# Performance work log

Measured on AMD Instinct MI355X. Metric: run time of the kernel, lower is better.

The kernel has to match this reference:

```python
import jax, jax.numpy as jnp
import numpy as np

EPS = 1e-15
FEAT = 128
HALF = FEAT // 2
N_RBF = 20
CUTOFF = 5.0
NUM_CONV = 3
N_ATOMS = 10000
N_EDGES = 160000
N_Z = 100


def setup_inputs() -> dict:
    key = jax.random.key(0)
    ks = iter(jax.random.split(key, 40))

    def W(shape):
        fan_in = shape[-2] if len(shape) > 1 else 1
        return (jax.random.normal(next(ks), shape, jnp.float32) / np.sqrt(fan_in)).astype(jnp.float32)

    # graph
    xyz = jax.random.normal(next(ks), (N_ATOMS, 3), jnp.float32)
    z = jax.random.randint(next(ks), (N_ATOMS,), 0, N_Z)
    src = jax.random.randint(next(ks), (N_EDGES,), 0, N_ATOMS)
    off = jax.random.randint(next(ks), (N_EDGES,), 1, N_ATOMS)
    nbr_list = jnp.stack([src, (src + off) % N_ATOMS], axis=1)  # directed, no self-loops

    L = NUM_CONV
    inp = dict(
        xyz=xyz, z=z, nbr_list=nbr_list,
        embed=W((N_Z, FEAT)),
        msg_w1=W((L, FEAT, FEAT)), msg_b1=jnp.zeros((L, FEAT), jnp.float32),
        msg_w2=W((L, FEAT, 3 * FEAT)), msg_b2=jnp.zeros((L, 3 * FEAT), jnp.float32),
        dist_w=W((L, N_RBF, 3 * FEAT)), dist_b=jnp.zeros((L, 3 * FEAT), jnp.float32),
        upd_u=W((L, FEAT, FEAT)), upd_v=W((L, FEAT, FEAT)),
        upd_w1=W((L, 2 * FEAT, FEAT)), upd_b1=jnp.zeros((L, FEAT), jnp.float32),
        upd_w2=W((L, FEAT, 3 * FEAT)), upd_b2=jnp.zeros((L, 3 * FEAT), jnp.float32),
        ero_w1=W((FEAT, HALF)), ero_b1=jnp.zeros((HALF,), jnp.float32),
        ero_w2=W((HALF, 1)), ero_b2=jnp.zeros((1,), jnp.float32),
    )
    return inp


def _painn_forces(xyz, z, nbr_list, embed,
                  msg_w1, msg_b1, msg_w2, msg_b2, dist_w, dist_b,
                  upd_u, upd_v, upd_w1, upd_b1, upd_w2, upd_b2,
                  ero_w1, ero_b1, ero_w2, ero_b2):
    N = z.shape[0]
    i, j = nbr_list[:, 0], nbr_list[:, 1]
    r_ij = xyz[j] - xyz[i]                               # [E,3]
    dist = jnp.sqrt(jnp.sum(r_ij * r_ij + EPS, axis=-1))  # [E]
    unit = r_ij / dist[:, None]
    # radial basis: sin(n*pi*d/cutoff)/d, cosine cutoff envelope
    k_n = jnp.arange(1, N_RBF + 1, dtype=jnp.float32) * (np.pi / CUTOFF)
    rbf = jnp.sin(k_n * dist[:, None]) / dist[:, None]   # [E,n_rbf]
    env = jnp.where(dist < CUTOFF,
                    0.5 * (jnp.cos(np.pi * dist / CUTOFF) + 1.0), 0.0)  # [E]

    s = embed[z]                                         # [N,F]
    v = jnp.zeros((N, FEAT, 3), s.dtype)                 # [N,F,3]

    for l in range(NUM_CONV):
        # --- message block ---
        w_s = (rbf @ dist_w[l] + dist_b[l]) * env[:, None]                 # [E,3F]
        phi = jax.nn.silu(s @ msg_w1[l] + msg_b1[l]) @ msg_w2[l] + msg_b2[l]  # [N,3F]
        inv = (phi[j] * w_s).reshape(-1, 3, FEAT)                           # [E,3,F]
        dv_ij = inv[:, 0, :][..., None] * v[j] + inv[:, 2, :][..., None] * unit[:, None, :]
        ds_ij = inv[:, 1, :]
        s = s + jax.ops.segment_sum(ds_ij, i, num_segments=N)
        v = v + jax.ops.segment_sum(dv_ij, i, num_segments=N)
        # --- update block ---
        u_v = jnp.einsum('nfc,fg->ngc', v, upd_u[l])                        # [N,F,3]
        v_v = jnp.einsum('nfc,fg->ngc', v, upd_v[l])
        v_v_norm = jnp.sqrt(jnp.sum(v_v * v_v, axis=-1) + EPS)              # [N,F]
        s_stack = jnp.concatenate([s, v_v_norm], axis=-1)                   # [N,2F]
        sp = (jax.nn.silu(s_stack @ upd_w1[l] + upd_b1[l]) @ upd_w2[l] + upd_b2[l]).reshape(-1, 3, FEAT)
        v = v + u_v * sp[:, 0, :][..., None]
        s = s + jnp.sum(u_v * v_v, axis=-1) * sp[:, 1, :] + sp[:, 2, :]

    # --- edge readout -> per-atom forces ---
    e = s[i] + s[j]                                                         # [E,F]
    f_scalar = jax.nn.silu(e @ ero_w1 + ero_b1) @ ero_w2 + ero_b2           # [E,1]
    dis_vec = xyz[i] - xyz[j]
    dis = jnp.sqrt(jnp.sum(dis_vec * dis_vec, axis=1))[:, None]
    f_edge = f_scalar * (dis_vec / dis)                                     # [E,3]
    f_atom = (jax.ops.segment_sum(f_edge, i, num_segments=N)
              - jax.ops.segment_sum(f_edge, j, num_segments=N))             # [N,3]
    return f_atom


def reference(xyz, z, nbr_list, embed,
              msg_w1, msg_b1, msg_w2, msg_b2, dist_w, dist_b,
              upd_u, upd_v, upd_w1, upd_b1, upd_w2, upd_b2,
              ero_w1, ero_b1, ero_w2, ero_b2):
    return _painn_forces(xyz, z, nbr_list, embed,
                         msg_w1, msg_b1, msg_w2, msg_b2, dist_w, dist_b,
                         upd_u, upd_v, upd_w1, upd_b1, upd_w2, upd_b2,
                         ero_w1, ero_b1, ero_w2, ero_b2)
```

## Files before the change

### kernel.cpp

```cpp
#include <hip/hip_runtime.h>
#include <math.h>

#define EPS_F 1e-15f
#define NRBF 20
#define CUTOFF_F 5.0f
#define PI_F 3.14159265358979323846f

typedef unsigned short u16;
typedef _Float16 f16;
typedef f16 f16x8 __attribute__((ext_vector_type(8)));
typedef f16 f16x4 __attribute__((ext_vector_type(4)));
typedef f16 f16x2 __attribute__((ext_vector_type(2)));
typedef float floatx4 __attribute__((ext_vector_type(4)));

__device__ __forceinline__ float silu_f(float x) { return x / (1.0f + expf(-x)); }

__global__ __launch_bounds__(256) void hist_kernel(
    const int* __restrict__ nbr, int* __restrict__ hist, int E)
{
  int e = blockIdx.x * 256 + threadIdx.x;
  if (e >= E) return;
  atomicAdd(hist + nbr[2 * e], 1);
}

__global__ __launch_bounds__(1024) void scan_kernel(
    const int* __restrict__ hist, int* __restrict__ start,
    int* __restrict__ cursor, int N)
{
  __shared__ int wsum[16];
  __shared__ int carry_s;
  int tid = threadIdx.x;
  int lane = tid & 63, wid = tid >> 6;
  if (tid == 0) carry_s = 0;
  __syncthreads();
  for (int base = 0; base < N; base += 1024) {
    int x = (base + tid < N) ? hist[base + tid] : 0;
    int v = x;
#pragma unroll
    for (int o = 1; o < 64; o <<= 1) {
      int t2 = __shfl_up(v, o, 64);
      if (lane >= o) v += t2;
    }
    if (lane == 63) wsum[wid] = v;
    __syncthreads();
    if (tid < 16) {
      int w = wsum[tid];
#pragma unroll
      for (int o = 1; o < 16; o <<= 1) {
        int t2 = __shfl_up(w, o, 64);
        if (tid >= o) w += t2;
      }
      wsum[tid] = w;
    }
    __syncthreads();
    int wbase = (wid == 0) ? 0 : wsum[wid - 1];
    int incl = v + wbase;
    int carry = carry_s;
    if (base + tid < N) {
      int ex = carry + incl - x;
      start[base + tid] = ex;
      cursor[base + tid] = ex;
    }
    __syncthreads();
    if (tid == 1023) carry_s = carry + incl;
    __syncthreads();
  }
  if (tid == 0) start[N] = carry_s;
}

__global__ __launch_bounds__(256) void scatter_id_kernel(
    const int* __restrict__ nbr, int* __restrict__ cursor,
    int* __restrict__ order, int E)
{
  int e = blockIdx.x * 256 + threadIdx.x;
  if (e >= E) return;
  int pos = atomicAdd(cursor + nbr[2 * e], 1);
  order[pos] = e;
}

__global__ __launch_bounds__(256) void segsort_kernel(
    int* __restrict__ order, const int* __restrict__ start, int N)
{
  int wi = blockIdx.x * 4 + (threadIdx.x >> 6);
  int lane = threadIdx.x & 63;
  if (wi >= N) return;
  int s0 = start[wi], s1 = start[wi + 1];
  int len = s1 - s0;
  if (len <= 1) return;
  if (len <= 64) {
    int id = (lane < len) ? order[s0 + lane] : 0x7FFFFFFF;
    int rank = 0;
#pragma unroll
    for (int k = 0; k < 64; ++k) {
      int other = __shfl(id, k, 64);
      rank += (other < id) ? 1 : 0;
    }
    if (lane < len) order[s0 + rank] = id;
  } else if (lane == 0) {
    for (int a = s0 + 1; a < s1; ++a) {
      int key = order[a];
      int b = a - 1;
      while (b >= s0 && order[b] > key) { order[b + 1] = order[b]; --b; }
      order[b + 1] = key;
    }
  }
}

__global__ __launch_bounds__(256) void geom_fill_kernel(
    const int* __restrict__ order, const int* __restrict__ nbr,
    const float* __restrict__ xyz, int2* __restrict__ ij_s,
    float* __restrict__ unit_s, f16* __restrict__ rbf_h, int E)
{
  int p = blockIdx.x * 256 + threadIdx.x;
  if (p >= E) return;
  int e = order[p];
  int i = nbr[2 * e], j = nbr[2 * e + 1];
  float dx = xyz[3 * j + 0] - xyz[3 * i + 0];
  float dy = xyz[3 * j + 1] - xyz[3 * i + 1];
  float dz = xyz[3 * j + 2] - xyz[3 * i + 2];
  float d2 = dx * dx + dy * dy + dz * dz + 3.0f * EPS_F;
  float d = sqrtf(d2);
  float inv_d = 1.0f / d;
  ij_s[p] = make_int2(i, j);
  unit_s[3 * p + 0] = dx * inv_d;
  unit_s[3 * p + 1] = dy * inv_d;
  unit_s[3 * p + 2] = dz * inv_d;
  float x = d * (PI_F / CUTOFF_F);
  float s1, c1;
  __sincosf(x, &s1, &c1);
  float envv = (d < CUTOFF_F) ? 0.5f * (c1 + 1.0f) : 0.0f;
  f16 tmp[32];
  float two_c = 2.0f * c1;
  float env_inv_d = envv * inv_d;
  float sp = 0.0f, sn = s1;
  tmp[0] = (f16)(sn * env_inv_d);
#pragma unroll
  for (int n = 1; n < NRBF; ++n) {
    float nx = two_c * sn - sp;
    sp = sn; sn = nx;
    tmp[n] = (f16)(sn * env_inv_d);
  }
  tmp[NRBF] = (f16)envv;
#pragma unroll
  for (int n = NRBF + 1; n < 32; ++n) tmp[n] = (f16)0.0f;
#pragma unroll
  for (int g = 0; g < 4; ++g)
    *(f16x8*)(rbf_h + (size_t)p * 32 + g * 8) = *(f16x8*)&tmp[g * 8];
}

__global__ __launch_bounds__(256) void dwfrag_kernel(
    const float* __restrict__ dw, const float* __restrict__ db,
    f16* __restrict__ dwf)
{
  int idx = blockIdx.x * 256 + threadIdx.x;
  if (idx >= 3 * 24 * 64 * 8) return;
  int q = idx & 7;
  int lane = (idx >> 3) & 63;
  int ct = (idx >> 9) % 24;
  int l = idx / (24 * 64 * 8);
  int k = (lane >> 4) * 8 + q;
  int col = ct * 16 + (lane & 15);
  float val = 0.f;
  if (k < NRBF) val = dw[(size_t)l * NRBF * 384 + (size_t)k * 384 + col];
  else if (k == NRBF) val = db[(size_t)l * 384 + col];
  dwf[idx] = (f16)val;
}

__global__ __launch_bounds__(256) void embed_kernel(
    const int* __restrict__ z, const float* __restrict__ embed,
    float* __restrict__ s, f16* __restrict__ s_h, int N)
{
  int idx = blockIdx.x * 256 + threadIdx.x;
  if (idx >= N * 128) return;
  int n = idx >> 7, f = idx & 127;
  float x = embed[z[n] * 128 + f];
  s[idx] = x;
  s_h[idx] = (f16)x;
}

__global__ __launch_bounds__(256) void w1t_kernel(
    const float* __restrict__ w1, f16* __restrict__ w1t)
{
  int idx = blockIdx.x * 256 + threadIdx.x;
  if (idx >= 64 * 128) return;
  int n = idx >> 7, k = idx & 127;
  w1t[idx] = (f16)w1[(size_t)k * 64 + n];
}

template <bool SILU, int OUT, bool AH>
__global__ __launch_bounds__(256) void gemm_kernel(
    const void* __restrict__ Ap, const float* __restrict__ W,
    const float* __restrict__ bias, const float* __restrict__ rowscale,
    void* __restrict__ Cout, int M, int N, int K)
{
  __shared__ f16 As[64][40];
  __shared__ f16 Bs[64][40];
  int t = threadIdx.x;
  int wave = t >> 6, lane = t & 63;
  int rw = wave & 1, cw = wave >> 1;
  int lr = lane & 15, quad = lane >> 4;
  int row0 = blockIdx.x * 64, col0 = blockIdx.y * 64;
  floatx4 acc[2][2] = {};
  for (int k0 = 0; k0 < K; k0 += 32) {
    if (AH) {
      const f16* A = (const f16*)Ap;
      int sm = t >> 2, sk = (t & 3) * 8;
      f16x8 av;
      if (row0 + sm < M) av = *(const f16x8*)(A + (size_t)(row0 + sm) * K + k0 + sk);
      else { for (int q = 0; q < 8; ++q) av[q] = (f16)0.0f; }
      *(f16x8*)&As[sm][sk] = av;
    } else {
      const float* A = (const float*)Ap;
#pragma unroll
      for (int u0 = 0; u0 < 2; ++u0) {
        int u = t + u0 * 256;
        int m = u >> 3, c4 = (u & 7) * 4;
        float4 av = make_float4(0.f, 0.f, 0.f, 0.f);
        if (row0 + m < M) av = *(const float4*)(A + (size_t)(row0 + m) * K + k0 + c4);
        f16x4 hv;
        hv[0] = (f16)av.x; hv[1] = (f16)av.y; hv[2] = (f16)av.z; hv[3] = (f16)av.w;
        *(f16x4*)&As[m][c4] = hv;
      }
    }
#pragma unroll
    for (int u0 = 0; u0 < 2; ++u0) {
      int u = t + u0 * 256;
      int k = u >> 4, n4 = (u & 15) * 4;
      float4 wv = *(const float4*)(W + (size_t)(k0 + k) * N + col0 + n4);
      Bs[n4 + 0][k] = (f16)wv.x;
      Bs[n4 + 1][k] = (f16)wv.y;
      Bs[n4 + 2][k] = (f16)wv.z;
      Bs[n4 + 3][k] = (f16)wv.w;
    }
    __syncthreads();
    f16x8 af[2], bfr[2];
#pragma unroll
    for (int tr = 0; tr < 2; ++tr)
      af[tr] = *(const f16x8*)&As[rw * 32 + tr * 16 + lr][quad * 8];
#pragma unroll
    for (int tc = 0; tc < 2; ++tc)
      bfr[tc] = *(const f16x8*)&Bs[cw * 32 + tc * 16 + lr][quad * 8];
#pragma unroll
    for (int tr = 0; tr < 2; ++tr)
#pragma unroll
      for (int tc = 0; tc < 2; ++tc)
        acc[tr][tc] = __builtin_amdgcn_mfma_f32_16x16x32_f16(af[tr], bfr[tc], acc[tr][tc], 0, 0, 0);
    __syncthreads();
  }
#pragma unroll
  for (int tc = 0; tc < 2; ++tc) {
    int col = col0 + cw * 32 + tc * 16 + lr;
    float bb = bias ? bias[col] : 0.0f;
#pragma unroll
    for (int tr = 0; tr < 2; ++tr) {
#pragma unroll
      for (int r = 0; r < 4; ++r) {
        int row = row0 + rw * 32 + tr * 16 + quad * 4 + r;
        if (row < M) {
          float x = acc[tr][tc][r] + bb;
          if (rowscale) x *= rowscale[row];
          if (SILU) x = silu_f(x);
          size_t o = (size_t)row * N + col;
          if (OUT == 0) ((float*)Cout)[o] = x;
          else          ((f16*)Cout)[o] = (f16)x;
        }
      }
    }
  }
}

__global__ __launch_bounds__(256) void gemm_dual_kernel(
    const float* __restrict__ A, const float* __restrict__ W1,
    const float* __restrict__ W2, float* __restrict__ C1, float* __restrict__ C2,
    int M, int N, int K)
{
  __shared__ f16 As[64][40];
  __shared__ f16 Bs1[64][40];
  __shared__ f16 Bs2[64][40];
  int t = threadIdx.x;
  int wave = t >> 6, lane = t & 63;
  int rw = wave & 1, cw = wave >> 1;
  int lr = lane & 15, quad = lane >> 4;
  int row0 = blockIdx.x * 64, col0 = blockIdx.y * 64;
  floatx4 acc1[2][2] = {};
  floatx4 acc2[2][2] = {};
  for (int k0 = 0; k0 < K; k0 += 32) {
#pragma unroll
    for (int u0 = 0; u0 < 2; ++u0) {
      int u = t + u0 * 256;
      int m = u >> 3, c4 = (u & 7) * 4;
      float4 av = make_float4(0.f, 0.f, 0.f, 0.f);
      if (row0 + m < M) av = *(const float4*)(A + (size_t)(row0 + m) * K + k0 + c4);
      f16x4 hv;
      hv[0] = (f16)av.x; hv[1] = (f16)av.y; hv[2] = (f16)av.z; hv[3] = (f16)av.w;
      *(f16x4*)&As[m][c4] = hv;
    }
#pragma unroll
    for (int u0 = 0; u0 < 2; ++u0) {
      int u = t + u0 * 256;
      int k = u >> 4, n4 = (u & 15) * 4;
      float4 wv = *(const float4*)(W1 + (size_t)(k0 + k) * N + col0 + n4);
      Bs1[n4 + 0][k] = (f16)wv.x;
      Bs1[n4 + 1][k] = (f16)wv.y;
      Bs1[n4 + 2][k] = (f16)wv.z;
      Bs1[n4 + 3][k] = (f16)wv.w;
      float4 xv = *(const float4*)(W2 + (size_t)(k0 + k) * N + col0 + n4);
      Bs2[n4 + 0][k] = (f16)xv.x;
      Bs2[n4 + 1][k] = (f16)xv.y;
      Bs2[n4 + 2][k] = (f16)xv.z;
      Bs2[n4 + 3][k] = (f16)xv.w;
    }
    __syncthreads();
    f16x8 af[2], b1[2], b2[2];
#pragma unroll
    for (int tr = 0; tr < 2; ++tr)
      af[tr] = *(const f16x8*)&As[rw * 32 + tr * 16 + lr][quad * 8];
#pragma unroll
    for (int tc = 0; tc < 2; ++tc) {
      b1[tc] = *(const f16x8*)&Bs1[cw * 32 + tc * 16 + lr][quad * 8];
      b2[tc] = *(const f16x8*)&Bs2[cw * 32 + tc * 16 + lr][quad * 8];
    }
#pragma unroll
    for (int tr = 0; tr < 2; ++tr)
#pragma unroll
      for (int tc = 0; tc < 2; ++tc) {
        acc1[tr][tc] = __builtin_amdgcn_mfma_f32_16x16x32_f16(af[tr], b1[tc], acc1[tr][tc], 0, 0, 0);
        acc2[tr][tc] = __builtin_amdgcn_mfma_f32_16x16x32_f16(af[tr], b2[tc], acc2[tr][tc], 0, 0, 0);
      }
    __syncthreads();
  }
#pragma unroll
  for (int tc = 0; tc < 2; ++tc) {
    int col = col0 + cw * 32 + tc * 16 + lr;
#pragma unroll
    for (int tr = 0; tr < 2; ++tr) {
#pragma unroll
      for (int r = 0; r < 4; ++r) {
        int row = row0 + rw * 32 + tr * 16 + quad * 4 + r;
        if (row < M) {
          C1[(size_t)row * N + col] = acc1[tr][tc][r];
          C2[(size_t)row * N + col] = acc2[tr][tc][r];
        }
      }
    }
  }
}

#define MEPB 32
__global__ __launch_bounds__(384, 6) void message_kernel(
    const int2* __restrict__ ij_s, const float* __restrict__ unit_s,
    const f16* __restrict__ rbf_h, const f16* __restrict__ dwf,
    const f16* __restrict__ phi_h, const f16* __restrict__ vh,
    float* __restrict__ s, float* __restrict__ v, int E)
{
  __shared__ f16 rbfA[MEPB][40];
  __shared__ f16 wsT[384][38];
  __shared__ int2 ijL[MEPB];
  __shared__ float unitL[MEPB * 3];
  int t = threadIdx.x;
  int wave = t >> 6, lane = t & 63;
  int e_lo = blockIdx.x * MEPB;
  if (e_lo >= E) return;
  int e_hi = (e_lo + MEPB < E) ? e_lo + MEPB : E;
  int cnt = e_hi - e_lo;

  f16x8 bf[4];
#pragma unroll
  for (int i = 0; i < 4; ++i) {
    int ct = wave * 4 + i;
    bf[i] = *(const f16x8*)(dwf + ((size_t)ct * 64 + lane) * 8);
  }
  if (t < MEPB * 4) {
    int r = t >> 2, c8 = (t & 3) * 8;
    f16x8 rv;
    if (e_lo + r < E) rv = *(const f16x8*)(rbf_h + (size_t)(e_lo + r) * 32 + c8);
    else { for (int q = 0; q < 8; ++q) rv[q] = (f16)0.0f; }
    *(f16x8*)&rbfA[r][c8] = rv;
  }
  if (t < cnt) ijL[t] = ij_s[e_lo + t];
  if (t < cnt * 3) unitL[t] = unit_s[(size_t)e_lo * 3 + t];
  __syncthreads();

  int lr = lane & 15, quad = lane >> 4;
  f16x8 af[2];
#pragma unroll
  for (int tr = 0; tr < 2; ++tr)
    af[tr] = *(const f16x8*)&rbfA[tr * 16 + lr][quad * 8];
  floatx4 acc[2][4] = {};
#pragma unroll
  for (int tr = 0; tr < 2; ++tr)
#pragma unroll
    for (int i = 0; i < 4; ++i)
      acc[tr][i] = __builtin_amdgcn_mfma_f32_16x16x32_f16(af[tr], bf[i], acc[tr][i], 0, 0, 0);
#pragma unroll
  for (int tr = 0; tr < 2; ++tr)
#pragma unroll
    for (int i = 0; i < 4; ++i) {
      int col = (wave * 4 + i) * 16 + lr;
      int er = tr * 16 + quad * 4;
      f16x2 lo2, hi2;
      lo2[0] = (f16)acc[tr][i][0]; lo2[1] = (f16)acc[tr][i][1];
      hi2[0] = (f16)acc[tr][i][2]; hi2[1] = (f16)acc[tr][i][3];
      *(f16x2*)&wsT[col][er]     = lo2;
      *(f16x2*)&wsT[col][er + 2] = hi2;
    }
  __syncthreads();

  int g = t >> 7, f = t & 127;
  float a0 = 0.f, a1 = 0.f, a2 = 0.f;
  int prev_i = -1;
  f16 ph_0 = (f16)0.f, ph_1 = (f16)0.f, ph_2 = (f16)0.f, ph_3 = (f16)0.f;
  f16 ph_4 = (f16)0.f, ph_5 = (f16)0.f, ph_6 = (f16)0.f, ph_7 = (f16)0.f;
  f16 vj0_0 = (f16)0.f, vj1_0 = (f16)0.f, vj2_0 = (f16)0.f;
  f16 vj0_1 = (f16)0.f, vj1_1 = (f16)0.f, vj2_1 = (f16)0.f;
  f16 vj0_2 = (f16)0.f, vj1_2 = (f16)0.f, vj2_2 = (f16)0.f;
  f16 vj0_3 = (f16)0.f, vj1_3 = (f16)0.f, vj2_3 = (f16)0.f;
  f16 vj0_4 = (f16)0.f, vj1_4 = (f16)0.f, vj2_4 = (f16)0.f;
  f16 vj0_5 = (f16)0.f, vj1_5 = (f16)0.f, vj2_5 = (f16)0.f;
  f16 vj0_6 = (f16)0.f, vj1_6 = (f16)0.f, vj2_6 = (f16)0.f;
  f16 vj0_7 = (f16)0.f, vj1_7 = (f16)0.f, vj2_7 = (f16)0.f;

#define MK_LOAD(S, RR) do { int rv_ = (RR); if (rv_ < cnt) {                  \
    int jj_ = ijL[rv_].y;                                                      \
    ph_##S = phi_h[(size_t)jj_ * 384 + t];                                     \
    if (g == 0) { const f16* vp_ = vh + (size_t)jj_ * 384 + f;                 \
      vj0_##S = vp_[0]; vj1_##S = vp_[128]; vj2_##S = vp_[256]; }              \
  } } while (0)

#define MK_PROC(S, RR) do { int rv_ = (RR); if (rv_ < cnt) {                   \
    int ix_ = ijL[rv_].x;                                                      \
    if (ix_ != prev_i) {                                                       \
      if (prev_i >= 0) {                                                       \
        if (g == 1) atomicAdd(s + (size_t)prev_i * 128 + f, a0);               \
        else { float* vb_ = v + (size_t)prev_i * 384 + f;                      \
          atomicAdd(vb_, a0); atomicAdd(vb_ + 128, a1); atomicAdd(vb_ + 256, a2); } \
        a0 = a1 = a2 = 0.f; }                                                  \
      prev_i = ix_; }                                                          \
    float ws_ = (float)wsT[t][rv_];                                            \
    float inv_ = (float)ph_##S * ws_;                                          \
    if (g == 0) { a0 = fmaf(inv_, (float)vj0_##S, a0);                         \
                  a1 = fmaf(inv_, (float)vj1_##S, a1);                         \
                  a2 = fmaf(inv_, (float)vj2_##S, a2); }                       \
    else if (g == 1) { a0 += inv_; }                                           \
    else { a0 = fmaf(inv_, unitL[3 * rv_ + 0], a0);                            \
           a1 = fmaf(inv_, unitL[3 * rv_ + 1], a1);                            \
           a2 = fmaf(inv_, unitL[3 * rv_ + 2], a2); }                          \
  } } while (0)

  MK_LOAD(0, 0); MK_LOAD(1, 1); MK_LOAD(2, 2); MK_LOAD(3, 3);
  MK_LOAD(4, 4); MK_LOAD(5, 5); MK_LOAD(6, 6); MK_LOAD(7, 7);
  for (int r = 0; r < cnt; r += 8) {
    MK_PROC(0, r);     MK_LOAD(0, r + 8);
    MK_PROC(1, r + 1); MK_LOAD(1, r + 9);
    MK_PROC(2, r + 2); MK_LOAD(2, r + 10);
    MK_PROC(3, r + 3); MK_LOAD(3, r + 11);
    MK_PROC(4, r + 4); MK_LOAD(4, r + 12);
    MK_PROC(5, r + 5); MK_LOAD(5, r + 13);
    MK_PROC(6, r + 6); MK_LOAD(6, r + 14);
    MK_PROC(7, r + 7); MK_LOAD(7, r + 15);
  }
#undef MK_LOAD
#undef MK_PROC
  if (prev_i >= 0) {
    if (g == 1) {
      atomicAdd(s + (size_t)prev_i * 128 + f, a0);
    } else {
      float* vb = v + (size_t)prev_i * 384 + f;
      atomicAdd(vb, a0);
      atomicAdd(vb + 128, a1);
      atomicAdd(vb + 256, a2);
    }
  }
}

__global__ __launch_bounds__(256) void stack_kernel(
    const float* __restrict__ s, const float* __restrict__ v_v,
    f16* __restrict__ s_stack, int N)
{
  int idx = blockIdx.x * 256 + threadIdx.x;
  if (idx >= N * 128) return;
  int n = idx >> 7, g = idx & 127;
  float a = v_v[(size_t)n * 384 + g];
  float b = v_v[(size_t)n * 384 + 128 + g];
  float c = v_v[(size_t)n * 384 + 256 + g];
  s_stack[(size_t)n * 256 + g] = (f16)s[idx];
  s_stack[(size_t)n * 256 + 128 + g] = (f16)sqrtf(a * a + b * b + c * c + EPS_F);
}

__global__ __launch_bounds__(256) void apply_kernel(
    float* __restrict__ s, f16* __restrict__ s_h,
    float* __restrict__ v, f16* __restrict__ v_h,
    const float* __restrict__ u_v, const float* __restrict__ v_v,
    const float* __restrict__ sp, int N)
{
  int idx = blockIdx.x * 256 + threadIdx.x;
  if (idx >= N * 128) return;
  int n = idx >> 7, g = idx & 127;
  float sp0 = sp[(size_t)n * 384 + g];
  float sp1 = sp[(size_t)n * 384 + 128 + g];
  float sp2 = sp[(size_t)n * 384 + 256 + g];
  float dot = 0.f;
#pragma unroll
  for (int c = 0; c < 3; ++c) {
    size_t o = (size_t)n * 384 + c * 128 + g;
    float uv = u_v[o];
    float vn = fmaf(uv, sp0, v[o]);
    v[o] = vn;
    v_h[o] = (f16)vn;
    dot = fmaf(uv, v_v[o], dot);
  }
  float sn = s[idx] + dot * sp1 + sp2;
  s[idx] = sn;
  s_h[idx] = (f16)sn;
}

__global__ __launch_bounds__(256) void readout_gemm_kernel(
    const int* __restrict__ nbr, const float* __restrict__ xyz,
    const f16* __restrict__ s_h, const f16* __restrict__ w1t,
    const float* __restrict__ b1, const float* __restrict__ w2,
    const float* __restrict__ b2, float* __restrict__ out, int E)
{
  __shared__ f16 As[64][40];
  __shared__ f16 Bs[64][40];
  __shared__ float red[2][64];
  __shared__ int ijc[64][2];
  int t = threadIdx.x;
  int wave = t >> 6, lane = t & 63;
  int rw = wave & 1, cw = wave >> 1;
  int lr = lane & 15, quad = lane >> 4;
  int e0b = blockIdx.x * 64;
  if (t < 64) {
    int e = e0b + t;
    if (e < E) { ijc[t][0] = nbr[2 * e]; ijc[t][1] = nbr[2 * e + 1]; }
    else { ijc[t][0] = 0; ijc[t][1] = 0; }
  }
  __syncthreads();
  int m = t >> 2;
  int c8 = (t & 3) * 8;
  int im = ijc[m][0], jm = ijc[m][1];
  bool okm = (e0b + m) < E;
  f16x8 xa[4], ya[4];
  if (okm) {
#pragma unroll
    for (int w = 0; w < 4; ++w) {
      xa[w] = *(const f16x8*)(s_h + (size_t)im * 128 + w * 32 + c8);
      ya[w] = *(const f16x8*)(s_h + (size_t)jm * 128 + w * 32 + c8);
    }
  } else {
#pragma unroll
    for (int w = 0; w < 4; ++w)
      for (int q = 0; q < 8; ++q) { xa[w][q] = (f16)0.0f; ya[w][q] = (f16)0.0f; }
  }
  floatx4 acc[2][2] = {};
#pragma unroll
  for (int w = 0; w < 4; ++w) {
    *(f16x8*)&As[m][c8] = xa[w] + ya[w];
    {
      int sm = t >> 2, sk = (t & 3) * 8;
      *(f16x8*)&Bs[sm][sk] = *(const f16x8*)(w1t + (size_t)sm * 128 + w * 32 + sk);
    }
    __syncthreads();
    f16x8 af[2], bfr[2];
#pragma unroll
    for (int tr = 0; tr < 2; ++tr)
      af[tr] = *(const f16x8*)&As[rw * 32 + tr * 16 + lr][quad * 8];
#pragma unroll
    for (int tc = 0; tc < 2; ++tc)
      bfr[tc] = *(const f16x8*)&Bs[cw * 32 + tc * 16 + lr][quad * 8];
#pragma unroll
    for (int tr = 0; tr < 2; ++tr)
#pragma unroll
      for (int tc = 0; tc < 2; ++tc)
        acc[tr][tc] = __builtin_amdgcn_mfma_f32_16x16x32_f16(af[tr], bfr[tc], acc[tr][tc], 0, 0, 0);
    __syncthreads();
  }
  float b1v[2], w2v[2];
#pragma unroll
  for (int tc = 0; tc < 2; ++tc) {
    int col = cw * 32 + tc * 16 + lr;
    b1v[tc] = b1[col];
    w2v[tc] = w2[col];
  }
#pragma unroll
  for (int tr = 0; tr < 2; ++tr) {
#pragma unroll
    for (int r = 0; r < 4; ++r) {
      float p = 0.f;
#pragma unroll
      for (int tc = 0; tc < 2; ++tc)
        p += silu_f(acc[tr][tc][r] + b1v[tc]) * w2v[tc];
#pragma unroll
      for (int ofs = 1; ofs < 16; ofs <<= 1) p += __shfl_xor(p, ofs, 64);
      if (lr == 0) red[cw][rw * 32 + tr * 16 + quad * 4 + r] = p;
    }
  }
  __syncthreads();
  if (t < 64) {
    int e = e0b + t;
    if (e < E) {
      float fs = red[0][t] + red[1][t] + b2[0];
      int i = ijc[t][0], j = ijc[t][1];
      float dx = xyz[3 * i + 0] - xyz[3 * j + 0];
      float dy = xyz[3 * i + 1] - xyz[3 * j + 1];
      float dz = xyz[3 * i + 2] - xyz[3 * j + 2];
      float dis = sqrtf(dx * dx + dy * dy + dz * dz);
      float sc = fs / dis;
      float fx = sc * dx, fy = sc * dy, fz = sc * dz;
      atomicAdd(out + (size_t)i * 3 + 0, fx);
      atomicAdd(out + (size_t)i * 3 + 1, fy);
      atomicAdd(out + (size_t)i * 3 + 2, fz);
      atomicAdd(out + (size_t)j * 3 + 0, -fx);
      atomicAdd(out + (size_t)j * 3 + 1, -fy);
      atomicAdd(out + (size_t)j * 3 + 2, -fz);
    }
  }
}

extern "C" void kernel_launch(void* const* d_in, const int* in_sizes, int n_in,
                              void* d_out, int out_size, void* d_ws, size_t ws_size,
                              hipStream_t stream) {
  const float* xyz    = (const float*)d_in[0];
  const int*   z      = (const int*)d_in[1];
  const int*   nbr    = (const int*)d_in[2];
  const float* embed  = (const float*)d_in[3];
  const float* msg_w1 = (const float*)d_in[4];
  const float* msg_b1 = (const float*)d_in[5];
  const float* msg_w2 = (const float*)d_in[6];
  const float* msg_b2 = (const float*)d_in[7];
  const float* dist_w = (const float*)d_in[8];
  const float* dist_b = (const float*)d_in[9];
  const float* upd_u  = (const float*)d_in[10];
  const float* upd_v  = (const float*)d_in[11];
  const float* upd_w1 = (const float*)d_in[12];
  const float* upd_b1 = (const float*)d_in[13];
  const float* upd_w2 = (const float*)d_in[14];
  const float* upd_b2 = (const float*)d_in[15];
  const float* ero_w1 = (const float*)d_in[16];
  const float* ero_b1 = (const float*)d_in[17];
  const float* ero_w2 = (const float*)d_in[18];
  const float* ero_b2 = (const float*)d_in[19];

  const int N = in_sizes[1];
  const int E = in_sizes[2] / 2;
  const int L = 3;

  char* ws = (char*)d_ws;
  size_t off = 0;
  auto alloc = [&](size_t bytes) -> void* {
    void* p = ws + off;
    off += (bytes + 255) & ~(size_t)255;
    return p;
  };
  float* unit_s = (float*)alloc((size_t)E * 3 * 4);
  f16*   rbf_h  = (f16*)alloc((size_t)E * 32 * 2);
  int2*  ij_s   = (int2*)alloc((size_t)E * 8);
  int*   order  = (int*)alloc((size_t)E * 4);
  float* s      = (float*)alloc((size_t)N * 128 * 4);
  f16*   s_h    = (f16*)alloc((size_t)N * 128 * 2);
  float* vA     = (float*)alloc((size_t)N * 384 * 4);
  f16*   vhA    = (f16*)alloc((size_t)N * 384 * 2);
  f16*   phi_h  = (f16*)alloc((size_t)N * 384 * 2);
  f16*   w1t    = (f16*)alloc((size_t)64 * 128 * 2);
  f16*   dwf    = (f16*)alloc((size_t)3 * 24 * 64 * 8 * 2);
  int*   histx  = (int*)alloc((size_t)(N + 1) * 4);
  int*   startp = (int*)alloc((size_t)(N + 1) * 4);
  int*   cursor = (int*)alloc((size_t)N * 4);
  float* u_v    = (float*)alloc((size_t)N * 384 * 4);
  float* v_v    = (float*)alloc((size_t)N * 384 * 4);
  float* sp     = (float*)alloc((size_t)N * 384 * 4);
  f16*   sstk_h = (f16*)alloc((size_t)N * 256 * 2);
  f16*   h_h    = (f16*)alloc((size_t)N * 128 * 2);

  auto cdiv = [](int a, int b) { return (a + b - 1) / b; };

  hipMemsetAsync(vA, 0, (size_t)N * 384 * 4, stream);
  hipMemsetAsync(vhA, 0, (size_t)N * 384 * 2, stream);
  hipMemsetAsync(histx, 0, (size_t)(N + 1) * 4, stream);
  hist_kernel<<<cdiv(E, 256), 256, 0, stream>>>(nbr, histx, E);
  scan_kernel<<<1, 1024, 0, stream>>>(histx, startp, cursor, N);
  scatter_id_kernel<<<cdiv(E, 256), 256, 0, stream>>>(nbr, cursor, order, E);
  segsort_kernel<<<cdiv(N, 4), 256, 0, stream>>>(order, startp, N);
  geom_fill_kernel<<<cdiv(E, 256), 256, 0, stream>>>(
      order, nbr, xyz, ij_s, unit_s, rbf_h, E);
  embed_kernel<<<cdiv(N * 128, 256), 256, 0, stream>>>(z, embed, s, s_h, N);
  w1t_kernel<<<cdiv(64 * 128, 256), 256, 0, stream>>>(ero_w1, w1t);
  dwfrag_kernel<<<cdiv(3 * 24 * 64 * 8, 256), 256, 0, stream>>>(dist_w, dist_b, dwf);

  for (int l = 0; l < L; ++l) {
    gemm_kernel<true, 1, true><<<dim3(cdiv(N, 64), 2), 256, 0, stream>>>(
        s_h, msg_w1 + (size_t)l * 128 * 128, msg_b1 + (size_t)l * 128, nullptr, h_h, N, 128, 128);
    gemm_kernel<false, 1, true><<<dim3(cdiv(N, 64), 6), 256, 0, stream>>>(
        h_h, msg_w2 + (size_t)l * 128 * 384, msg_b2 + (size_t)l * 384, nullptr, phi_h, N, 384, 128);
    message_kernel<<<cdiv(E, MEPB), 384, 0, stream>>>(
        ij_s, unit_s, rbf_h, dwf + (size_t)l * 24 * 64 * 8,
        phi_h, vhA, s, vA, E);
    gemm_dual_kernel<<<dim3(cdiv(N * 3, 64), 2), 256, 0, stream>>>(
        vA, upd_u + (size_t)l * 128 * 128, upd_v + (size_t)l * 128 * 128,
        u_v, v_v, N * 3, 128, 128);
    stack_kernel<<<cdiv(N * 128, 256), 256, 0, stream>>>(s, v_v, sstk_h, N);
    gemm_kernel<true, 1, true><<<dim3(cdiv(N, 64), 2), 256, 0, stream>>>(
        sstk_h, upd_w1 + (size_t)l * 256 * 128, upd_b1 + (size_t)l * 128, nullptr, h_h, N, 128, 256);
    gemm_kernel<false, 0, true><<<dim3(cdiv(N, 64), 6), 256, 0, stream>>>(
        h_h, upd_w2 + (size_t)l * 128 * 384, upd_b2 + (size_t)l * 384, nullptr, sp, N, 384, 128);
    apply_kernel<<<cdiv(N * 128, 256), 256, 0, stream>>>(
        s, s_h, vA, vhA, u_v, v_v, sp, N);
  }

  hipMemsetAsync(d_out, 0, (size_t)out_size * 4, stream);
  readout_gemm_kernel<<<cdiv(E, 64), 256, 0, stream>>>(
      nbr, xyz, s_h, w1t, ero_b1, ero_w2, ero_b2, (float*)d_out, E);
}
```

Baseline: 718.5 us.

## Fuse two-layer MLP GEMMs into one kernel keeping hidden activations in LDS

Replaces each pair of GEMM launches (Linear+SiLU, then Linear) with a single mlp_kernel per 64-row tile. The SiLU hidden layer stays in shared memory, so the f16 hidden buffer is no longer written to or read from global memory, and two launches per layer are removed. The cost is that each block now loops over all 384 output columns serially with less parallelism (157 blocks instead of 314-940) and uses more shared memory. Message kernel occupancy hint is also lowered from 6 to 4.

```diff
diff --git a/kernel.cpp b/kernel.cpp
--- a/kernel.cpp
+++ b/kernel.cpp
@@ -187,82 +187,115 @@
   w1t[idx] = (f16)w1[(size_t)k * 64 + n];
 }
 
-template <bool SILU, int OUT, bool AH>
-__global__ __launch_bounds__(256) void gemm_kernel(
-    const void* __restrict__ Ap, const float* __restrict__ W,
-    const float* __restrict__ bias, const float* __restrict__ rowscale,
-    void* __restrict__ Cout, int M, int N, int K)
+template <int K1, int OUT>
+__global__ __launch_bounds__(256) void mlp_kernel(
+    const f16* __restrict__ A, const float* __restrict__ W1,
+    const float* __restrict__ b1, const float* __restrict__ W2,
+    const float* __restrict__ b2, void* __restrict__ Cout, int M)
 {
   __shared__ f16 As[64][40];
-  __shared__ f16 Bs[64][40];
+  __shared__ f16 Bs1[128][40];
+  __shared__ f16 hs[64][136];
   int t = threadIdx.x;
   int wave = t >> 6, lane = t & 63;
-  int rw = wave & 1, cw = wave >> 1;
   int lr = lane & 15, quad = lane >> 4;
-  int row0 = blockIdx.x * 64, col0 = blockIdx.y * 64;
-  floatx4 acc[2][2] = {};
-  for (int k0 = 0; k0 < K; k0 += 32) {
-    if (AH) {
-      const f16* A = (const f16*)Ap;
+  int row0 = blockIdx.x * 64;
+
+  floatx4 acc_h[4][2] = {};
+  for (int k0 = 0; k0 < K1; k0 += 32) {
+    {
       int sm = t >> 2, sk = (t & 3) * 8;
       f16x8 av;
-      if (row0 + sm < M) av = *(const f16x8*)(A + (size_t)(row0 + sm) * K + k0 + sk);
+      if (row0 + sm < M) av = *(const f16x8*)(A + (size_t)(row0 + sm) * K1 + k0 + sk);
       else { for (int q = 0; q < 8; ++q) av[q] = (f16)0.0f; }
       *(f16x8*)&As[sm][sk] = av;
-    } else {
-      const float* A = (const float*)Ap;
+    }
+#pragma unroll
+    for (int u0 = 0; u0 < 4; ++u0) {
+      int u = t + u0 * 256;
+      int k = u >> 5;
+      int c4 = (u & 31) * 4;
+      float4 wv = *(const float4*)(W1 + (size_t)(k0 + k) * 128 + c4);
+      Bs1[c4 + 0][k] = (f16)wv.x;
+      Bs1[c4 + 1][k] = (f16)wv.y;
+      Bs1[c4 + 2][k] = (f16)wv.z;
+      Bs1[c4 + 3][k] = (f16)wv.w;
+    }
+    __syncthreads();
+    f16x8 af[4], bfr[2];
+#pragma unroll
+    for (int tr = 0; tr < 4; ++tr)
+      af[tr] = *(const f16x8*)&As[tr * 16 + lr][quad * 8];
+#pragma unroll
+    for (int tc = 0; tc < 2; ++tc)
+      bfr[tc] = *(const f16x8*)&Bs1[wave * 32 + tc * 16 + lr][quad * 8];
+#pragma unroll
+    for (int tr = 0; tr < 4; ++tr)
+#pragma unroll
+      for (int tc = 0; tc < 2; ++tc)
+        acc_h[tr][tc] = __builtin_amdgcn_mfma_f32_16x16x32_f16(af[tr], bfr[tc], acc_h[tr][tc], 0, 0, 0);
+    __syncthreads();
+  }
+#pragma unroll
+  for (int tc = 0; tc < 2; ++tc) {
+    int col = wave * 32 + tc * 16 + lr;
+    float bb = b1[col];
+#pragma unroll
+    for (int tr = 0; tr < 4; ++tr) {
+#pragma unroll
+      for (int r = 0; r < 4; ++r) {
+        int row = tr * 16 + quad * 4 + r;
+        hs[row][col] = (f16)silu_f(acc_h[tr][tc][r] + bb);
+      }
+    }
+  }
+  __syncthreads();
+
+  int rw = wave & 1, cw = wave >> 1;
+  for (int chunk = 0; chunk < 6; ++chunk) {
+    int c0 = chunk * 64;
+    floatx4 acc[2][2] = {};
+    for (int k0 = 0; k0 < 128; k0 += 32) {
 #pragma unroll
       for (int u0 = 0; u0 < 2; ++u0) {
         int u = t + u0 * 256;
-        int m = u >> 3, c4 = (u & 7) * 4;
-        float4 av = make_float4(0.f, 0.f, 0.f, 0.f);
-        if (row0 + m < M) av = *(const float4*)(A + (size_t)(row0 + m) * K + k0 + c4);
-        f16x4 hv;
-        hv[0] = (f16)av.x; hv[1] = (f16)av.y; hv[2] = (f16)av.z; hv[3] = (f16)av.w;
-        *(f16x4*)&As[m][c4] = hv;
+        int k = u >> 4, n4 = (u & 15) * 4;
+        float4 wv = *(const float4*)(W2 + (size_t)(k0 + k) * 384 + c0 + n4);
+        Bs1[n4 + 0][k] = (f16)wv.x;
+        Bs1[n4 + 1][k] = (f16)wv.y;
+        Bs1[n4 + 2][k] = (f16)wv.z;
+        Bs1[n4 + 3][k] = (f16)wv.w;
       }
-    }
-#pragma unroll
-    for (int u0 = 0; u0 < 2; ++u0) {
-      int u = t + u0 * 256;
-      int k = u >> 4, n4 = (u & 15) * 4;
-      float4 wv = *(const float4*)(W + (size_t)(k0 + k) * N + col0 + n4);
-      Bs[n4 + 0][k] = (f16)wv.x;
-      Bs[n4 + 1][k] = (f16)wv.y;
-      Bs[n4 + 2][k] = (f16)wv.z;
-      Bs[n4 + 3][k] = (f16)wv.w;
-    }
-    __syncthreads();
-    f16x8 af[2], bfr[2];
-#pragma unroll
-    for (int tr = 0; tr < 2; ++tr)
-      af[tr] = *(const f16x8*)&As[rw * 32 + tr * 16 + lr][quad * 8];
-#pragma unroll
-    for (int tc = 0; tc < 2; ++tc)
-      bfr[tc] = *(const f16x8*)&Bs[cw * 32 + tc * 16 + lr][quad * 8];
-#pragma unroll
-    for (int tr = 0; tr < 2; ++tr)
+      __syncthreads();
+      f16x8 af[2], bfr[2];
+#pragma unroll
+      for (int tr = 0; tr < 2; ++tr)
+        af[tr] = *(const f16x8*)&hs[rw * 32 + tr * 16 + lr][k0 + quad * 8];
 #pragma unroll
       for (int tc = 0; tc < 2; ++tc)
-        acc[tr][tc] = __builtin_amdgcn_mfma_f32_16x16x32_f16(af[tr], bfr[tc], acc[tr][tc], 0, 0, 0);
-    __syncthreads();
-  }
-#pragma unroll
-  for (int tc = 0; tc < 2; ++tc) {
-    int col = col0 + cw * 32 + tc * 16 + lr;
-    float bb = bias ? bias[col] : 0.0f;
-#pragma unroll
-    for (int tr = 0; tr < 2; ++tr) {
-#pragma unroll
-      for (int r = 0; r < 4; ++r) {
-        int row = row0 + rw * 32 + tr * 16 + quad * 4 + r;
-        if (row < M) {
-          float x = acc[tr][tc][r] + bb;
-          if (rowscale) x *= rowscale[row];
-          if (SILU) x = silu_f(x);
-          size_t o = (size_t)row * N + col;
-          if (OUT == 0) ((float*)Cout)[o] = x;
-          else          ((f16*)Cout)[o] = (f16)x;
+        bfr[tc] = *(const f16x8*)&Bs1[cw * 32 + tc * 16 + lr][quad * 8];
+#pragma unroll
+      for (int tr = 0; tr < 2; ++tr)
+#pragma unroll
+        for (int tc = 0; tc < 2; ++tc)
+          acc[tr][tc] = __builtin_amdgcn_mfma_f32_16x16x32_f16(af[tr], bfr[tc], acc[tr][tc], 0, 0, 0);
+      __syncthreads();
+    }
+#pragma unroll
+    for (int tc = 0; tc < 2; ++tc) {
+      int col = c0 + cw * 32 + tc * 16 + lr;
+      float bb = b2[col];
+#pragma unroll
+      for (int tr = 0; tr < 2; ++tr) {
+#pragma unroll
+        for (int r = 0; r < 4; ++r) {
+          int row = row0 + rw * 32 + tr * 16 + quad * 4 + r;
+          if (row < M) {
+            float x = acc[tr][tc][r] + bb;
+            size_t o = (size_t)row * 384 + col;
+            if (OUT == 0) ((float*)Cout)[o] = x;
+            else          ((f16*)Cout)[o] = (f16)x;
+          }
         }
       }
     }
@@ -347,7 +380,7 @@
 }
 
 #define MEPB 32
-__global__ __launch_bounds__(384, 6) void message_kernel(
+__global__ __launch_bounds__(384, 4) void message_kernel(
     const int2* __restrict__ ij_s, const float* __restrict__ unit_s,
     const f16* __restrict__ rbf_h, const f16* __restrict__ dwf,
     const f16* __restrict__ phi_h, const f16* __restrict__ vh,
@@ -669,7 +702,6 @@
   float* v_v    = (float*)alloc((size_t)N * 384 * 4);
   float* sp     = (float*)alloc((size_t)N * 384 * 4);
   f16*   sstk_h = (f16*)alloc((size_t)N * 256 * 2);
-  f16*   h_h    = (f16*)alloc((size_t)N * 128 * 2);
 
   auto cdiv = [](int a, int b) { return (a + b - 1) / b; };
 
@@ -687,10 +719,9 @@
   dwfrag_kernel<<<cdiv(3 * 24 * 64 * 8, 256), 256, 0, stream>>>(dist_w, dist_b, dwf);
 
   for (int l = 0; l < L; ++l) {
-    gemm_kernel<true, 1, true><<<dim3(cdiv(N, 64), 2), 256, 0, stream>>>(
-        s_h, msg_w1 + (size_t)l * 128 * 128, msg_b1 + (size_t)l * 128, nullptr, h_h, N, 128, 128);
-    gemm_kernel<false, 1, true><<<dim3(cdiv(N, 64), 6), 256, 0, stream>>>(
-        h_h, msg_w2 + (size_t)l * 128 * 384, msg_b2 + (size_t)l * 384, nullptr, phi_h, N, 384, 128);
+    mlp_kernel<128, 1><<<cdiv(N, 64), 256, 0, stream>>>(
+        s_h, msg_w1 + (size_t)l * 128 * 128, msg_b1 + (size_t)l * 128,
+        msg_w2 + (size_t)l * 128 * 384, msg_b2 + (size_t)l * 384, phi_h, N);
     message_kernel<<<cdiv(E, MEPB), 384, 0, stream>>>(
         ij_s, unit_s, rbf_h, dwf + (size_t)l * 24 * 64 * 8,
         phi_h, vhA, s, vA, E);
@@ -698,10 +729,9 @@
         vA, upd_u + (size_t)l * 128 * 128, upd_v + (size_t)l * 128 * 128,
         u_v, v_v, N * 3, 128, 128);
     stack_kernel<<<cdiv(N * 128, 256), 256, 0, stream>>>(s, v_v, sstk_h, N);
-    gemm_kernel<true, 1, true><<<dim3(cdiv(N, 64), 2), 256, 0, stream>>>(
-        sstk_h, upd_w1 + (size_t)l * 256 * 128, upd_b1 + (size_t)l * 128, nullptr, h_h, N, 128, 256);
-    gemm_kernel<false, 0, true><<<dim3(cdiv(N, 64), 6), 256, 0, stream>>>(
-        h_h, upd_w2 + (size_t)l * 128 * 384, upd_b2 + (size_t)l * 384, nullptr, sp, N, 384, 128);
+    mlp_kernel<256, 0><<<cdiv(N, 64), 256, 0, stream>>>(
+        sstk_h, upd_w1 + (size_t)l * 256 * 128, upd_b1 + (size_t)l * 128,
+        upd_w2 + (size_t)l * 128 * 384, upd_b2 + (size_t)l * 384, sp, N);
     apply_kernel<<<cdiv(N * 128, 256), 256, 0, stream>>>(
         s, s_h, vA, vhA, u_v, v_v, sp, N);
   }
```

New measurement: 834.3 us. 1.16x slower.
